# Optimization experiments

Hardware: AMD Instinct MI355X
Metric: run time of the kernel (lower is better)

## Reference

```python
import jax, jax.numpy as jnp
import numpy as np

ATT_PROP = 2  # config['att_prop']
NEG_BIAS = 1e23


def _bucket(d):
    # standard coref-style distance bucketing into 10 buckets
    d = jnp.abs(d)
    return jnp.where(d <= 4, d,
           jnp.where(d <= 7, 5,
           jnp.where(d <= 15, 6,
           jnp.where(d <= 31, 7,
           jnp.where(d <= 63, 8, 9))))).astype(jnp.int32)


def setup_inputs() -> dict:
    key = jax.random.key(0)
    ks = jax.random.split(key, 12)
    B, N, M, D, H = 2, 1024, 2048, 512, 64
    scale = 0.02  # init_weights_std

    update = jax.random.normal(ks[0], (B, N, D), jnp.float32)
    span_begin = jnp.sort(jax.random.randint(ks[1], (B, N), 0, 2000), axis=-1).astype(jnp.int32)
    span_end = (span_begin + jax.random.randint(ks[2], (B, N), 0, 10)).astype(jnp.int32)
    square_mask = jnp.ones((B, N, N), jnp.float32)
    cand_span_vecs = jax.random.normal(ks[3], (B, M, D), jnp.float32)
    # unique prune indices per batch (a pruned span maps to one candidate slot)
    prune_indices_hoi = jnp.stack([
        jnp.sort(jax.random.permutation(jax.random.fold_in(ks[4], b), M)[:N])
        for b in range(B)]).astype(jnp.int32)
    span_lengths = jnp.array([900, 1024], dtype=jnp.int32)

    W_left = jax.random.normal(ks[5], (D, H), jnp.float32) * scale
    W_right = jax.random.normal(ks[6], (D, H), jnp.float32) * scale
    b_h = jnp.zeros((H,), jnp.float32)
    dist_emb = jax.random.normal(ks[7], (10, H), jnp.float32) * scale
    v_out = jax.random.normal(ks[8], (H,), jnp.float32) * scale
    b_out = jnp.zeros((), jnp.float32)
    W_gate = jax.random.normal(ks[9], (2 * D, D), jnp.float32) * scale
    b_gate = jnp.zeros((D,), jnp.float32)

    return dict(update=update, square_mask=square_mask, cand_span_vecs=cand_span_vecs,
                span_begin=span_begin, span_end=span_end,
                prune_indices_hoi=prune_indices_hoi, span_lengths=span_lengths,
                W_left=W_left, W_right=W_right, b_h=b_h, dist_emb=dist_emb,
                v_out=v_out, b_out=b_out, W_gate=W_gate, b_gate=b_gate)


def reference(update, square_mask, cand_span_vecs, span_begin, span_end,
              prune_indices_hoi, span_lengths, W_left, W_right, b_h,
              dist_emb, v_out, b_out, W_gate, b_gate):
    B, N, D = update.shape
    # pairwise distance features are iteration-invariant: precompute once
    dist = dist_emb[_bucket(span_begin[:, :, None] - span_begin[:, None, :])]  # [B,N,N,H]
    bias = -(1.0 - square_mask) * NEG_BIAS  # [B,N,N]

    for _ in range(ATT_PROP):
        left = update @ W_left    # [B,N,H]
        right = update @ W_right  # [B,N,H]
        h = jax.nn.relu(left[:, :, None, :] + right[:, None, :, :] + dist + b_h)  # [B,N,N,H]
        scores = jnp.einsum('bijh,h->bij', h, v_out) + b_out  # [B,N,N]
        probs = jax.nn.softmax(scores + bias, axis=-1)
        ctxt = jnp.einsum('bij,bjd->bid', probs, update)  # [B,N,D]
        g = jax.nn.sigmoid(jnp.concatenate([update, ctxt], axis=-1) @ W_gate + b_gate)
        update = g * update + (1.0 - g) * ctxt

    # overwrite_spans_hoi: scatter first span_lengths[b] updated vectors back
    valid = jnp.arange(N) < span_lengths[:, None]  # [B,N]

    def scatter_one(cand, idx, upd, m):
        cur = cand[idx]  # [N,D]
        vals = jnp.where(m[:, None], upd, cur)  # invalid rows write back original
        return cand.at[idx].set(vals)

    cand_new = jax.vmap(scatter_one)(cand_span_vecs, prune_indices_hoi, update, valid)
    return cand_new, update
```

## Files before the change

kernel.cpp:

```cpp
#include <hip/hip_runtime.h>
#include <cstdint>

#define NB 2
#define NN 1024
#define MM 2048
#define DD 512
#define HH 64
#define ST 68
#define STB 72

typedef __attribute__((ext_vector_type(8))) short bf16x8;
typedef __attribute__((ext_vector_type(4))) float f32x4;

__device__ inline ushort f2bf(float x) {
  union { float f; uint32_t u; } v; v.f = x;
  uint32_t u = v.u;
  u += 0x7FFF + ((u >> 16) & 1);
  return (ushort)(u >> 16);
}
__device__ inline float bflo(uint32_t d) { return __uint_as_float(d << 16); }
__device__ inline float bfhi(uint32_t d) { return __uint_as_float(d & 0xFFFF0000u); }

#define GLDS(gp, lp) \
  __builtin_amdgcn_global_load_lds( \
      (const __attribute__((address_space(1))) void*)(gp), \
      (__attribute__((address_space(3))) void*)(lp), 16, 0, 0)

__global__ __launch_bounds__(256) void lr_kernel(
    const float* __restrict__ U, const float* __restrict__ Wl,
    const float* __restrict__ Wr, float* __restrict__ left,
    ushort* __restrict__ right_bf) {
  __shared__ float u[8][DD];
  const int block = blockIdx.x;
  const int tid = threadIdx.x;
  const float4* Uv = (const float4*)(U + (size_t)block * 8 * DD);
  float4* uv = (float4*)&u[0][0];
#pragma unroll
  for (int t = 0; t < 4; ++t) uv[tid + t * 256] = Uv[tid + t * 256];
  __syncthreads();
  const int h = tid & 63;
  const int isR = (tid >> 6) & 1;
  const int rbase = tid >> 7;
  const float* __restrict__ W = isR ? Wr : Wl;
  float acc[4] = {0.f, 0.f, 0.f, 0.f};
  for (int k0 = 0; k0 < DD; k0 += 4) {
    float w0 = W[(k0 + 0) * HH + h];
    float w1 = W[(k0 + 1) * HH + h];
    float w2 = W[(k0 + 2) * HH + h];
    float w3 = W[(k0 + 3) * HH + h];
#pragma unroll
    for (int r = 0; r < 4; ++r) {
      float4 u4 = *(const float4*)&u[rbase + r * 2][k0];
      acc[r] = fmaf(u4.w, w3, fmaf(u4.z, w2, fmaf(u4.y, w1, fmaf(u4.x, w0, acc[r]))));
    }
  }
  if (isR) {
#pragma unroll
    for (int r = 0; r < 4; ++r)
      right_bf[(size_t)(block * 8 + rbase + r * 2) * HH + h] = f2bf(acc[r]);
  } else {
#pragma unroll
    for (int r = 0; r < 4; ++r)
      left[(size_t)(block * 8 + rbase + r * 2) * HH + h] = acc[r];
  }
}

__global__ __launch_bounds__(256) void conv_t(
    const float* __restrict__ in, ushort* __restrict__ out_row,
    ushort* __restrict__ out_T, int R, int C, int write_row) {
  __shared__ float tile[64][65];
  const int b = blockIdx.z;
  const int r0 = blockIdx.y * 64, c0 = blockIdx.x * 64;
  const int tx = threadIdx.x & 15, ty = threadIdx.x >> 4;
  const float* inb = in + (size_t)b * R * C;
#pragma unroll
  for (int p = 0; p < 4; ++p) {
    const int r = ty + p * 16;
    const float4 v = *(const float4*)&inb[(size_t)(r0 + r) * C + c0 + tx * 4];
    tile[r][tx * 4 + 0] = v.x; tile[r][tx * 4 + 1] = v.y;
    tile[r][tx * 4 + 2] = v.z; tile[r][tx * 4 + 3] = v.w;
    if (write_row) {
      ushort4 o = make_ushort4(f2bf(v.x), f2bf(v.y), f2bf(v.z), f2bf(v.w));
      *(ushort4*)&out_row[(size_t)b * R * C + (size_t)(r0 + r) * C + c0 + tx * 4] = o;
    }
  }
  __syncthreads();
  ushort* oT = out_T + (size_t)b * R * C;
#pragma unroll
  for (int p = 0; p < 4; ++p) {
    const int rr = ty + p * 16;
    ushort4 o;
    o.x = f2bf(tile[tx * 4 + 0][rr]);
    o.y = f2bf(tile[tx * 4 + 1][rr]);
    o.z = f2bf(tile[tx * 4 + 2][rr]);
    o.w = f2bf(tile[tx * 4 + 3][rr]);
    *(ushort4*)&oT[(size_t)(c0 + rr) * R + r0 + tx * 4] = o;
  }
}

__global__ __launch_bounds__(256) void score_softmax(
    const float* __restrict__ left, const ushort* __restrict__ right_bf,
    const int* __restrict__ span_begin, const float* __restrict__ mask,
    const float* __restrict__ dist_emb, const float* __restrict__ b_h,
    const float* __restrict__ v_out, ushort* __restrict__ probs_bf) {
  __shared__ ushort Rt[64][STB];
  __shared__ ushort LDb[4][10][STB];
  __shared__ float Dbh[10][ST];
  __shared__ float Lt[4][ST];
  __shared__ float Sc[4][NN];
  __shared__ int sbj[NN];
  const int b = blockIdx.y;
  const int r0 = blockIdx.x * 4;
  const int tid = threadIdx.x;
  const int wave = tid >> 6, lane = tid & 63;
  const int row = r0 + wave;

  for (int f = tid; f < 160; f += 256) {
    int bk = f >> 4, h4 = f & 15;
    float4 d = *(const float4*)&dist_emb[bk * HH + h4 * 4];
    float4 bh = *(const float4*)&b_h[h4 * 4];
    d.x += bh.x; d.y += bh.y; d.z += bh.z; d.w += bh.w;
    *(float4*)&Dbh[bk][h4 * 4] = d;
  }
  if (tid < 64) {
    int r = tid >> 4, h4 = tid & 15;
    *(float4*)&Lt[r][h4 * 4] =
        *(const float4*)&left[((size_t)b * NN + r0 + r) * HH + h4 * 4];
  }
  for (int t = tid; t < NN; t += 256) sbj[t] = span_begin[b * NN + t];
  __syncthreads();
  for (int f = tid; f < 2560; f += 256) {
    int i = f >> 9;
    i = f / 640;
    int rem = f - i * 640;
    int bk = rem >> 6, h = rem & 63;
    LDb[i][bk][h] = f2bf(Lt[i][h] + Dbh[bk][h]);
  }
  float4 vr[16];
#pragma unroll
  for (int hq = 0; hq < 16; ++hq) vr[hq] = *(const float4*)&v_out[hq * 4];
  const int my_sbi = span_begin[(size_t)b * NN + row];
  const float* maskrow = mask + ((size_t)b * NN + row) * NN;

#pragma unroll 1
  for (int c = 0; c < 16; ++c) {
    __syncthreads();
#pragma unroll
    for (int t = 0; t < 2; ++t) {
      const int f = tid + t * 256;
      const int r = f >> 3, u8 = f & 7;
      *(bf16x8*)&Rt[r][u8 * 8] =
          *(const bf16x8*)&right_bf[((size_t)b * NN + c * 64 + r) * HH + u8 * 8];
    }
    __syncthreads();
    int d = sbj[c * 64 + lane] - my_sbi;
    d = d < 0 ? -d : d;
    const int bk =
        d <= 4 ? d : (d <= 7 ? 5 : (d <= 15 ? 6 : (d <= 31 ? 7 : (d <= 63 ? 8 : 9))));
    const ushort* zp = &LDb[wave][bk][0];
    const ushort* rp = &Rt[lane][0];
    float acc = 0.f;
#pragma unroll
    for (int oct = 0; oct < 8; ++oct) {
      const uint4 zd = *(const uint4*)&zp[oct * 8];
      const uint4 rd = *(const uint4*)&rp[oct * 8];
      const float4 v0 = vr[2 * oct], v1 = vr[2 * oct + 1];
      acc = fmaf(fmaxf(bflo(zd.x) + bflo(rd.x), 0.f), v0.x, acc);
      acc = fmaf(fmaxf(bfhi(zd.x) + bfhi(rd.x), 0.f), v0.y, acc);
      acc = fmaf(fmaxf(bflo(zd.y) + bflo(rd.y), 0.f), v0.z, acc);
      acc = fmaf(fmaxf(bfhi(zd.y) + bfhi(rd.y), 0.f), v0.w, acc);
      acc = fmaf(fmaxf(bflo(zd.z) + bflo(rd.z), 0.f), v1.x, acc);
      acc = fmaf(fmaxf(bfhi(zd.z) + bfhi(rd.z), 0.f), v1.y, acc);
      acc = fmaf(fmaxf(bflo(zd.w) + bflo(rd.w), 0.f), v1.z, acc);
      acc = fmaf(fmaxf(bfhi(zd.w) + bfhi(rd.w), 0.f), v1.w, acc);
    }
    const float mval = maskrow[c * 64 + lane];
    Sc[wave][c * 64 + lane] = acc - (1.0f - mval) * 1e23f;
  }
  float mx = -3.0e38f;
#pragma unroll
  for (int c = 0; c < 16; ++c) mx = fmaxf(mx, Sc[wave][c * 64 + lane]);
#pragma unroll
  for (int off = 32; off; off >>= 1) mx = fmaxf(mx, __shfl_xor(mx, off));
  float sum = 0.f;
#pragma unroll
  for (int c = 0; c < 16; ++c) {
    const float e = __expf(Sc[wave][c * 64 + lane] - mx);
    Sc[wave][c * 64 + lane] = e;
    sum += e;
  }
#pragma unroll
  for (int off = 32; off; off >>= 1) sum += __shfl_xor(sum, off);
  const float inv = 1.0f / sum;
  ushort* prow = probs_bf + ((size_t)b * NN + row) * NN;
#pragma unroll
  for (int c = 0; c < 16; ++c)
    prow[c * 64 + lane] = f2bf(Sc[wave][c * 64 + lane] * inv);
}

__global__ __launch_bounds__(256) void gemm_ctxt_mfma(
    const ushort* __restrict__ Pbf, const ushort* __restrict__ UT,
    ushort* __restrict__ Cbf) {
  __shared__ ushort As[64 * 64];
  __shared__ ushort Bs[64 * 64];
  const int b = blockIdx.z;
  const int m0 = blockIdx.y * 64, n0 = blockIdx.x * 64;
  const int tid = threadIdx.x;
  const int lane = tid & 63, wave = tid >> 6;
  const int wm = (wave >> 1) * 32, wn = (wave & 1) * 32;
  const ushort* Ab = Pbf + (size_t)b * NN * NN;
  const ushort* Bb = UT + (size_t)b * DD * NN;
  f32x4 acc[2][2] = {};
  const int fm = lane & 15, quad = lane >> 4;
  for (int k0 = 0; k0 < NN; k0 += 64) {
#pragma unroll
    for (int t = 0; t < 2; ++t) {
      const int idx = tid + t * 256;
      const int r = idx >> 3, c8 = idx & 7;
      const int g = c8 ^ (r & 7);
      GLDS(Ab + (size_t)(m0 + r) * NN + k0 + g * 8, As + idx * 8);
      GLDS(Bb + (size_t)(n0 + r) * NN + k0 + g * 8, Bs + idx * 8);
    }
    __syncthreads();
#pragma unroll
    for (int s = 0; s < 2; ++s) {
      bf16x8 af[2], bfr[2];
#pragma unroll
      for (int tm = 0; tm < 2; ++tm) {
        const int row = wm + tm * 16 + fm;
        const int c8 = (s * 4 + quad) ^ (row & 7);
        af[tm] = *(const bf16x8*)&As[row * 64 + c8 * 8];
      }
#pragma unroll
      for (int tn = 0; tn < 2; ++tn) {
        const int row = wn + tn * 16 + fm;
        const int c8 = (s * 4 + quad) ^ (row & 7);
        bfr[tn] = *(const bf16x8*)&Bs[row * 64 + c8 * 8];
      }
#pragma unroll
      for (int tm = 0; tm < 2; ++tm)
#pragma unroll
        for (int tn = 0; tn < 2; ++tn)
          acc[tm][tn] = __builtin_amdgcn_mfma_f32_16x16x32_bf16(
              af[tm], bfr[tn], acc[tm][tn], 0, 0, 0);
    }
    __syncthreads();
  }
#pragma unroll
  for (int tm = 0; tm < 2; ++tm)
#pragma unroll
    for (int tn = 0; tn < 2; ++tn) {
      const int col = n0 + wn + tn * 16 + fm;
#pragma unroll
      for (int r = 0; r < 4; ++r) {
        const int row = m0 + wm + tm * 16 + quad * 4 + r;
        Cbf[(size_t)b * NN * DD + (size_t)row * DD + col] = f2bf(acc[tm][tn][r]);
      }
    }
}

__global__ __launch_bounds__(256) void gemm_gate_mfma(
    const ushort* __restrict__ Ubf, const ushort* __restrict__ Cbf,
    const ushort* __restrict__ WgT, const float* __restrict__ bg,
    const float* __restrict__ Uf, float* __restrict__ Uout,
    ushort* __restrict__ UbfOut, ushort* __restrict__ UTOut) {
  __shared__ ushort As[64 * 64];
  __shared__ ushort Bs[64 * 64];
  __shared__ ushort Tt[64][66];
  const int b = blockIdx.z;
  const int m0 = blockIdx.y * 64, n0 = blockIdx.x * 64;
  const int tid = threadIdx.x;
  const int lane = tid & 63, wave = tid >> 6;
  const int wm = (wave >> 1) * 32, wn = (wave & 1) * 32;
  f32x4 acc[2][2] = {};
  const int fm = lane & 15, quad = lane >> 4;
  for (int k0 = 0; k0 < 2 * DD; k0 += 64) {
    const ushort* Abase = (k0 < DD) ? (Ubf + (size_t)b * NN * DD)
                                    : (Cbf + (size_t)b * NN * DD);
    const int kc = k0 & (DD - 1);
#pragma unroll
    for (int t = 0; t < 2; ++t) {
      const int idx = tid + t * 256;
      const int r = idx >> 3, c8 = idx & 7;
      const int g = c8 ^ (r & 7);
      GLDS(Abase + (size_t)(m0 + r) * DD + kc + g * 8, As + idx * 8);
      GLDS(WgT + (size_t)(n0 + r) * (2 * DD) + k0 + g * 8, Bs + idx * 8);
    }
    __syncthreads();
#pragma unroll
    for (int s = 0; s < 2; ++s) {
      bf16x8 af[2], bfr[2];
#pragma unroll
      for (int tm = 0; tm < 2; ++tm) {
        const int row = wm + tm * 16 + fm;
        const int c8 = (s * 4 + quad) ^ (row & 7);
        af[tm] = *(const bf16x8*)&As[row * 64 + c8 * 8];
      }
#pragma unroll
      for (int tn = 0; tn < 2; ++tn) {
        const int row = wn + tn * 16 + fm;
        const int c8 = (s * 4 + quad) ^ (row & 7);
        bfr[tn] = *(const bf16x8*)&Bs[row * 64 + c8 * 8];
      }
#pragma unroll
      for (int tm = 0; tm < 2; ++tm)
#pragma unroll
        for (int tn = 0; tn < 2; ++tn)
          acc[tm][tn] = __builtin_amdgcn_mfma_f32_16x16x32_bf16(
              af[tm], bfr[tn], acc[tm][tn], 0, 0, 0);
    }
    __syncthreads();
  }
#pragma unroll
  for (int tm = 0; tm < 2; ++tm)
#pragma unroll
    for (int tn = 0; tn < 2; ++tn) {
      const int cl = wn + tn * 16 + fm;
      const int col = n0 + cl;
      const float bgv = bg[col];
#pragma unroll
      for (int r = 0; r < 4; ++r) {
        const int rl = wm + tm * 16 + quad * 4 + r;
        const int row = m0 + rl;
        const size_t off = (size_t)b * NN * DD + (size_t)row * DD + col;
        const float g = 1.f / (1.f + __expf(-(acc[tm][tn][r] + bgv)));
        const float cv = __uint_as_float(((uint32_t)Cbf[off]) << 16);
        const float o = g * Uf[off] + (1.f - g) * cv;
        Uout[off] = o;
        const ushort ob = f2bf(o);
        UbfOut[off] = ob;
        Tt[rl][cl] = ob;
      }
    }
  __syncthreads();
#pragma unroll
  for (int p = 0; p < 4; ++p) {
    const int cl = (tid >> 4) + p * 16;
    const int rl = (tid & 15) * 4;
    ushort4 o;
    o.x = Tt[rl + 0][cl]; o.y = Tt[rl + 1][cl];
    o.z = Tt[rl + 2][cl]; o.w = Tt[rl + 3][cl];
    *(ushort4*)&UTOut[((size_t)b * DD + n0 + cl) * NN + m0 + rl] = o;
  }
}

__global__ __launch_bounds__(256) void out_copy(
    const float* __restrict__ cand, const float* __restrict__ upd,
    float* __restrict__ out) {
  const int t = blockIdx.x * 256 + threadIdx.x;
  float4* o4 = (float4*)out;
  if (t < 524288) o4[t] = ((const float4*)cand)[t];
  else o4[t] = ((const float4*)upd)[t - 524288];
}

__global__ __launch_bounds__(128) void scatter_k(
    float* __restrict__ out_cand, const float* __restrict__ upd,
    const int* __restrict__ prune, const int* __restrict__ span_len) {
  const int row = blockIdx.x;
  const int b = row >> 10, i = row & 1023;
  if (i >= span_len[b]) return;
  const int dst = prune[row];
  const float4* src = (const float4*)(upd + (size_t)row * DD);
  float4* d = (float4*)(out_cand + ((size_t)b * MM + dst) * DD);
  d[threadIdx.x] = src[threadIdx.x];
}

extern "C" void kernel_launch(void* const* d_in, const int* in_sizes, int n_in,
                              void* d_out, int out_size, void* d_ws, size_t ws_size,
                              hipStream_t stream) {
  const float* update = (const float*)d_in[0];
  const float* mask = (const float*)d_in[1];
  const float* cand = (const float*)d_in[2];
  const int* span_begin = (const int*)d_in[3];
  const int* prune = (const int*)d_in[5];
  const int* span_len = (const int*)d_in[6];
  const float* Wl = (const float*)d_in[7];
  const float* Wr = (const float*)d_in[8];
  const float* b_h = (const float*)d_in[9];
  const float* dist_emb = (const float*)d_in[10];
  const float* v_out = (const float*)d_in[11];
  const float* Wg = (const float*)d_in[13];
  const float* b_gate = (const float*)d_in[14];

  char* w = (char*)d_ws;
  float* left = (float*)w;        w += (size_t)NB * NN * HH * 4;
  ushort* right_bf = (ushort*)w;  w += (size_t)NB * NN * HH * 2;
  ushort* probs_bf = (ushort*)w;  w += (size_t)NB * NN * NN * 2;
  ushort* ctxt_bf = (ushort*)w;   w += (size_t)NB * NN * DD * 2;
  float* upd1 = (float*)w;        w += (size_t)NB * NN * DD * 4;
  float* upd2 = (float*)w;        w += (size_t)NB * NN * DD * 4;
  ushort* Ubf0 = (ushort*)w;      w += (size_t)NB * NN * DD * 2;
  ushort* Ubf1 = (ushort*)w;      w += (size_t)NB * NN * DD * 2;
  ushort* UT = (ushort*)w;        w += (size_t)NB * NN * DD * 2;
  ushort* WgT = (ushort*)w;       w += (size_t)2 * DD * DD * 2;

  float* out = (float*)d_out;

  conv_t<<<dim3(8, 16, 1), 256, 0, stream>>>(Wg, WgT, WgT, 2 * DD, DD, 0);
  conv_t<<<dim3(8, 16, NB), 256, 0, stream>>>(update, Ubf0, UT, NN, DD, 1);

  const float* Ucur = update;
  float* nexts[2] = {upd1, upd2};
  ushort* ubf_in[2] = {Ubf0, Ubf1};
  ushort* ubf_out[2] = {Ubf1, Ubf0};
  for (int it = 0; it < 2; ++it) {
    lr_kernel<<<256, 256, 0, stream>>>(Ucur, Wl, Wr, left, right_bf);
    score_softmax<<<dim3(NN / 4, NB), 256, 0, stream>>>(
        left, right_bf, span_begin, mask, dist_emb, b_h, v_out, probs_bf);
    gemm_ctxt_mfma<<<dim3(8, 16, NB), 256, 0, stream>>>(probs_bf, UT, ctxt_bf);
    gemm_gate_mfma<<<dim3(8, 16, NB), 256, 0, stream>>>(
        ubf_in[it], ctxt_bf, WgT, b_gate, Ucur, nexts[it], ubf_out[it], UT);
    Ucur = nexts[it];
  }
  out_copy<<<3072, 256, 0, stream>>>(cand, Ucur, out);
  scatter_k<<<NB * NN, 128, 0, stream>>>(out, Ucur, prune, span_len);
}
```

Before: 240.1 us.

## Fuse all stages into one persistent kernel with software grid barriers

Replaces the sequence of separate launches (transpose/convert, left-right projection, score softmax, context GEMM, gate GEMM, copy, scatter) with a single persistent kernel of 512 blocks that walks the phases and separates them with an atomic-counter grid barrier. The aim is to remove per-launch overhead and the idle gaps between small kernels. The candidate copy is overlapped with the first projection phase, and the score dot product is split into two accumulators for more instruction-level parallelism. In exchange, all 512 blocks must be co-resident for the barrier to avoid deadlock, the GEMM phases use only 256 of the 512 blocks, and each barrier costs spinning on atomics.

Result: slower. 913.8 us (+280.6%).

```diff
diff --git a/kernel.cpp b/kernel.cpp
--- a/kernel.cpp
+++ b/kernel.cpp
@@ -8,6 +8,7 @@
 #define HH 64
 #define ST 68
 #define STB 72
+#define GRID 512
 
 typedef __attribute__((ext_vector_type(8))) short bf16x8;
 typedef __attribute__((ext_vector_type(4))) float f32x4;
@@ -26,66 +27,52 @@
       (const __attribute__((address_space(1))) void*)(gp), \
       (__attribute__((address_space(3))) void*)(lp), 16, 0, 0)
 
-__global__ __launch_bounds__(256) void lr_kernel(
-    const float* __restrict__ U, const float* __restrict__ Wl,
-    const float* __restrict__ Wr, float* __restrict__ left,
-    ushort* __restrict__ right_bf) {
-  __shared__ float u[8][DD];
-  const int block = blockIdx.x;
-  const int tid = threadIdx.x;
-  const float4* Uv = (const float4*)(U + (size_t)block * 8 * DD);
-  float4* uv = (float4*)&u[0][0];
-#pragma unroll
-  for (int t = 0; t < 4; ++t) uv[tid + t * 256] = Uv[tid + t * 256];
-  __syncthreads();
-  const int h = tid & 63;
-  const int isR = (tid >> 6) & 1;
-  const int rbase = tid >> 7;
-  const float* __restrict__ W = isR ? Wr : Wl;
-  float acc[4] = {0.f, 0.f, 0.f, 0.f};
-  for (int k0 = 0; k0 < DD; k0 += 4) {
-    float w0 = W[(k0 + 0) * HH + h];
-    float w1 = W[(k0 + 1) * HH + h];
-    float w2 = W[(k0 + 2) * HH + h];
-    float w3 = W[(k0 + 3) * HH + h];
-#pragma unroll
-    for (int r = 0; r < 4; ++r) {
-      float4 u4 = *(const float4*)&u[rbase + r * 2][k0];
-      acc[r] = fmaf(u4.w, w3, fmaf(u4.z, w2, fmaf(u4.y, w1, fmaf(u4.x, w0, acc[r]))));
-    }
-  }
-  if (isR) {
-#pragma unroll
-    for (int r = 0; r < 4; ++r)
-      right_bf[(size_t)(block * 8 + rbase + r * 2) * HH + h] = f2bf(acc[r]);
-  } else {
-#pragma unroll
-    for (int r = 0; r < 4; ++r)
-      left[(size_t)(block * 8 + rbase + r * 2) * HH + h] = acc[r];
-  }
-}
-
-__global__ __launch_bounds__(256) void conv_t(
-    const float* __restrict__ in, ushort* __restrict__ out_row,
-    ushort* __restrict__ out_T, int R, int C, int write_row) {
-  __shared__ float tile[64][65];
-  const int b = blockIdx.z;
-  const int r0 = blockIdx.y * 64, c0 = blockIdx.x * 64;
+struct KP {
+  const float *update, *mask, *cand;
+  const int *span_begin, *prune, *span_len;
+  const float *Wl, *Wr, *b_h, *dist_emb, *v_out, *Wg, *b_gate;
+  float *out;
+  int *bar;
+  float *left; ushort *right_bf; ushort *probs_bf; ushort *ctxt_bf;
+  float *upd1, *upd2; ushort *Ubf0, *Ubf1, *UT, *WgT;
+};
+
+__device__ inline void gsync(int* bar) {
+  __syncthreads();
+  __threadfence();
+  if (threadIdx.x == 0) {
+    int* cnt = bar;
+    int* gen = bar + 1;
+    const int g = atomicAdd(gen, 0);
+    if (atomicAdd(cnt, 1) == GRID - 1) {
+      atomicExch(cnt, 0);
+      __threadfence();
+      atomicAdd(gen, 1);
+    } else {
+      while (atomicAdd(gen, 0) == g) __builtin_amdgcn_s_sleep(2);
+    }
+    __threadfence();
+  }
+  __syncthreads();
+}
+
+__device__ void conv_tile(const float* __restrict__ in, ushort* out_row,
+                          ushort* __restrict__ out_T, int R, int C,
+                          int r0, int c0, char* smem) {
+  float (*tile)[65] = (float(*)[65])smem;
   const int tx = threadIdx.x & 15, ty = threadIdx.x >> 4;
-  const float* inb = in + (size_t)b * R * C;
 #pragma unroll
   for (int p = 0; p < 4; ++p) {
     const int r = ty + p * 16;
-    const float4 v = *(const float4*)&inb[(size_t)(r0 + r) * C + c0 + tx * 4];
+    const float4 v = *(const float4*)&in[(size_t)(r0 + r) * C + c0 + tx * 4];
     tile[r][tx * 4 + 0] = v.x; tile[r][tx * 4 + 1] = v.y;
     tile[r][tx * 4 + 2] = v.z; tile[r][tx * 4 + 3] = v.w;
-    if (write_row) {
+    if (out_row) {
       ushort4 o = make_ushort4(f2bf(v.x), f2bf(v.y), f2bf(v.z), f2bf(v.w));
-      *(ushort4*)&out_row[(size_t)b * R * C + (size_t)(r0 + r) * C + c0 + tx * 4] = o;
-    }
-  }
-  __syncthreads();
-  ushort* oT = out_T + (size_t)b * R * C;
+      *(ushort4*)&out_row[(size_t)(r0 + r) * C + c0 + tx * 4] = o;
+    }
+  }
+  __syncthreads();
 #pragma unroll
   for (int p = 0; p < 4; ++p) {
     const int rr = ty + p * 16;
@@ -94,53 +81,86 @@
     o.y = f2bf(tile[tx * 4 + 1][rr]);
     o.z = f2bf(tile[tx * 4 + 2][rr]);
     o.w = f2bf(tile[tx * 4 + 3][rr]);
-    *(ushort4*)&oT[(size_t)(c0 + rr) * R + r0 + tx * 4] = o;
-  }
-}
-
-__global__ __launch_bounds__(256) void score_softmax(
-    const float* __restrict__ left, const ushort* __restrict__ right_bf,
-    const int* __restrict__ span_begin, const float* __restrict__ mask,
-    const float* __restrict__ dist_emb, const float* __restrict__ b_h,
-    const float* __restrict__ v_out, ushort* __restrict__ probs_bf) {
-  __shared__ ushort Rt[64][STB];
-  __shared__ ushort LDb[4][10][STB];
-  __shared__ float Dbh[10][ST];
-  __shared__ float Lt[4][ST];
-  __shared__ float Sc[4][NN];
-  __shared__ int sbj[NN];
-  const int b = blockIdx.y;
-  const int r0 = blockIdx.x * 4;
+    *(ushort4*)&out_T[(size_t)(c0 + rr) * R + r0 + tx * 4] = o;
+  }
+  __syncthreads();
+}
+
+__device__ void lr_phase(const KP& P, const float* __restrict__ U, int vb,
+                         char* smem) {
+  float (*u)[DD] = (float(*)[DD])smem;
+  const int tid = threadIdx.x;
+  const float4* Uv = (const float4*)(U + (size_t)vb * 4 * DD);
+  float4* uv = (float4*)&u[0][0];
+#pragma unroll
+  for (int t = 0; t < 2; ++t) uv[tid + t * 256] = Uv[tid + t * 256];
+  __syncthreads();
+  const int h = tid & 63;
+  const int isR = (tid >> 6) & 1;
+  const int rsel = tid >> 7;
+  const float* __restrict__ W = isR ? P.Wr : P.Wl;
+  float acc[2] = {0.f, 0.f};
+  for (int k0 = 0; k0 < DD; k0 += 4) {
+    float w0 = W[(k0 + 0) * HH + h];
+    float w1 = W[(k0 + 1) * HH + h];
+    float w2 = W[(k0 + 2) * HH + h];
+    float w3 = W[(k0 + 3) * HH + h];
+#pragma unroll
+    for (int r = 0; r < 2; ++r) {
+      float4 u4 = *(const float4*)&u[rsel + r * 2][k0];
+      acc[r] = fmaf(u4.w, w3, fmaf(u4.z, w2, fmaf(u4.y, w1, fmaf(u4.x, w0, acc[r]))));
+    }
+  }
+  if (isR) {
+#pragma unroll
+    for (int r = 0; r < 2; ++r)
+      P.right_bf[(size_t)(vb * 4 + rsel + r * 2) * HH + h] = f2bf(acc[r]);
+  } else {
+#pragma unroll
+    for (int r = 0; r < 2; ++r)
+      P.left[(size_t)(vb * 4 + rsel + r * 2) * HH + h] = acc[r];
+  }
+  __syncthreads();
+}
+
+__device__ void score_phase(const KP& P, int vb, char* smem) {
+  ushort (*Rt)[STB] = (ushort(*)[STB])(smem);
+  ushort (*LDb)[10][STB] = (ushort(*)[10][STB])(smem + 9216);
+  float (*Dbh)[ST] = (float(*)[ST])(smem + 14976);
+  float (*Lt)[ST] = (float(*)[ST])(smem + 17696);
+  float (*Sc)[NN] = (float(*)[NN])(smem + 18784);
+  int* sbj = (int*)(smem + 35168);
+  const int b = vb >> 8;
+  const int r0 = (vb & 255) * 4;
   const int tid = threadIdx.x;
   const int wave = tid >> 6, lane = tid & 63;
   const int row = r0 + wave;
 
   for (int f = tid; f < 160; f += 256) {
     int bk = f >> 4, h4 = f & 15;
-    float4 d = *(const float4*)&dist_emb[bk * HH + h4 * 4];
-    float4 bh = *(const float4*)&b_h[h4 * 4];
+    float4 d = *(const float4*)&P.dist_emb[bk * HH + h4 * 4];
+    float4 bh = *(const float4*)&P.b_h[h4 * 4];
     d.x += bh.x; d.y += bh.y; d.z += bh.z; d.w += bh.w;
     *(float4*)&Dbh[bk][h4 * 4] = d;
   }
   if (tid < 64) {
     int r = tid >> 4, h4 = tid & 15;
     *(float4*)&Lt[r][h4 * 4] =
-        *(const float4*)&left[((size_t)b * NN + r0 + r) * HH + h4 * 4];
-  }
-  for (int t = tid; t < NN; t += 256) sbj[t] = span_begin[b * NN + t];
+        *(const float4*)&P.left[((size_t)b * NN + r0 + r) * HH + h4 * 4];
+  }
+  for (int t = tid; t < NN; t += 256) sbj[t] = P.span_begin[b * NN + t];
   __syncthreads();
   for (int f = tid; f < 2560; f += 256) {
-    int i = f >> 9;
-    i = f / 640;
+    int i = f / 640;
     int rem = f - i * 640;
     int bk = rem >> 6, h = rem & 63;
     LDb[i][bk][h] = f2bf(Lt[i][h] + Dbh[bk][h]);
   }
   float4 vr[16];
 #pragma unroll
-  for (int hq = 0; hq < 16; ++hq) vr[hq] = *(const float4*)&v_out[hq * 4];
-  const int my_sbi = span_begin[(size_t)b * NN + row];
-  const float* maskrow = mask + ((size_t)b * NN + row) * NN;
+  for (int hq = 0; hq < 16; ++hq) vr[hq] = *(const float4*)&P.v_out[hq * 4];
+  const int my_sbi = P.span_begin[(size_t)b * NN + row];
+  const float* maskrow = P.mask + ((size_t)b * NN + row) * NN;
 
 #pragma unroll 1
   for (int c = 0; c < 16; ++c) {
@@ -150,7 +170,7 @@
       const int f = tid + t * 256;
       const int r = f >> 3, u8 = f & 7;
       *(bf16x8*)&Rt[r][u8 * 8] =
-          *(const bf16x8*)&right_bf[((size_t)b * NN + c * 64 + r) * HH + u8 * 8];
+          *(const bf16x8*)&P.right_bf[((size_t)b * NN + c * 64 + r) * HH + u8 * 8];
     }
     __syncthreads();
     int d = sbj[c * 64 + lane] - my_sbi;
@@ -159,23 +179,38 @@
         d <= 4 ? d : (d <= 7 ? 5 : (d <= 15 ? 6 : (d <= 31 ? 7 : (d <= 63 ? 8 : 9))));
     const ushort* zp = &LDb[wave][bk][0];
     const ushort* rp = &Rt[lane][0];
-    float acc = 0.f;
-#pragma unroll
-    for (int oct = 0; oct < 8; ++oct) {
-      const uint4 zd = *(const uint4*)&zp[oct * 8];
-      const uint4 rd = *(const uint4*)&rp[oct * 8];
-      const float4 v0 = vr[2 * oct], v1 = vr[2 * oct + 1];
-      acc = fmaf(fmaxf(bflo(zd.x) + bflo(rd.x), 0.f), v0.x, acc);
-      acc = fmaf(fmaxf(bfhi(zd.x) + bfhi(rd.x), 0.f), v0.y, acc);
-      acc = fmaf(fmaxf(bflo(zd.y) + bflo(rd.y), 0.f), v0.z, acc);
-      acc = fmaf(fmaxf(bfhi(zd.y) + bfhi(rd.y), 0.f), v0.w, acc);
-      acc = fmaf(fmaxf(bflo(zd.z) + bflo(rd.z), 0.f), v1.x, acc);
-      acc = fmaf(fmaxf(bfhi(zd.z) + bfhi(rd.z), 0.f), v1.y, acc);
-      acc = fmaf(fmaxf(bflo(zd.w) + bflo(rd.w), 0.f), v1.z, acc);
-      acc = fmaf(fmaxf(bfhi(zd.w) + bfhi(rd.w), 0.f), v1.w, acc);
+    float acc0 = 0.f, acc1 = 0.f;
+#pragma unroll
+    for (int oct = 0; oct < 8; oct += 2) {
+      {
+        const uint4 zd = *(const uint4*)&zp[oct * 8];
+        const uint4 rd = *(const uint4*)&rp[oct * 8];
+        const float4 v0 = vr[2 * oct], v1 = vr[2 * oct + 1];
+        acc0 = fmaf(fmaxf(bflo(zd.x) + bflo(rd.x), 0.f), v0.x, acc0);
+        acc0 = fmaf(fmaxf(bfhi(zd.x) + bfhi(rd.x), 0.f), v0.y, acc0);
+        acc0 = fmaf(fmaxf(bflo(zd.y) + bflo(rd.y), 0.f), v0.z, acc0);
+        acc0 = fmaf(fmaxf(bfhi(zd.y) + bfhi(rd.y), 0.f), v0.w, acc0);
+        acc0 = fmaf(fmaxf(bflo(zd.z) + bflo(rd.z), 0.f), v1.x, acc0);
+        acc0 = fmaf(fmaxf(bfhi(zd.z) + bfhi(rd.z), 0.f), v1.y, acc0);
+        acc0 = fmaf(fmaxf(bflo(zd.w) + bflo(rd.w), 0.f), v1.z, acc0);
+        acc0 = fmaf(fmaxf(bfhi(zd.w) + bfhi(rd.w), 0.f), v1.w, acc0);
+      }
+      {
+        const uint4 zd = *(const uint4*)&zp[(oct + 1) * 8];
+        const uint4 rd = *(const uint4*)&rp[(oct + 1) * 8];
+        const float4 v0 = vr[2 * oct + 2], v1 = vr[2 * oct + 3];
+        acc1 = fmaf(fmaxf(bflo(zd.x) + bflo(rd.x), 0.f), v0.x, acc1);
+        acc1 = fmaf(fmaxf(bfhi(zd.x) + bfhi(rd.x), 0.f), v0.y, acc1);
+        acc1 = fmaf(fmaxf(bflo(zd.y) + bflo(rd.y), 0.f), v0.z, acc1);
+        acc1 = fmaf(fmaxf(bfhi(zd.y) + bfhi(rd.y), 0.f), v0.w, acc1);
+        acc1 = fmaf(fmaxf(bflo(zd.z) + bflo(rd.z), 0.f), v1.x, acc1);
+        acc1 = fmaf(fmaxf(bfhi(zd.z) + bfhi(rd.z), 0.f), v1.y, acc1);
+        acc1 = fmaf(fmaxf(bflo(zd.w) + bflo(rd.w), 0.f), v1.z, acc1);
+        acc1 = fmaf(fmaxf(bfhi(zd.w) + bfhi(rd.w), 0.f), v1.w, acc1);
+      }
     }
     const float mval = maskrow[c * 64 + lane];
-    Sc[wave][c * 64 + lane] = acc - (1.0f - mval) * 1e23f;
+    Sc[wave][c * 64 + lane] = (acc0 + acc1) - (1.0f - mval) * 1e23f;
   }
   float mx = -3.0e38f;
 #pragma unroll
@@ -192,24 +227,24 @@
 #pragma unroll
   for (int off = 32; off; off >>= 1) sum += __shfl_xor(sum, off);
   const float inv = 1.0f / sum;
-  ushort* prow = probs_bf + ((size_t)b * NN + row) * NN;
+  ushort* prow = P.probs_bf + ((size_t)b * NN + row) * NN;
 #pragma unroll
   for (int c = 0; c < 16; ++c)
     prow[c * 64 + lane] = f2bf(Sc[wave][c * 64 + lane] * inv);
-}
-
-__global__ __launch_bounds__(256) void gemm_ctxt_mfma(
-    const ushort* __restrict__ Pbf, const ushort* __restrict__ UT,
-    ushort* __restrict__ Cbf) {
-  __shared__ ushort As[64 * 64];
-  __shared__ ushort Bs[64 * 64];
-  const int b = blockIdx.z;
-  const int m0 = blockIdx.y * 64, n0 = blockIdx.x * 64;
+  __syncthreads();
+}
+
+__device__ void ctxt_phase(const KP& P, int vb, char* smem) {
+  ushort* As = (ushort*)smem;
+  ushort* Bs = (ushort*)(smem + 8192);
+  const int b = vb >> 7;
+  const int rem = vb & 127;
+  const int m0 = (rem >> 3) * 64, n0 = (rem & 7) * 64;
   const int tid = threadIdx.x;
   const int lane = tid & 63, wave = tid >> 6;
   const int wm = (wave >> 1) * 32, wn = (wave & 1) * 32;
-  const ushort* Ab = Pbf + (size_t)b * NN * NN;
-  const ushort* Bb = UT + (size_t)b * DD * NN;
+  const ushort* Ab = P.probs_bf + (size_t)b * NN * NN;
+  const ushort* Bb = P.UT + (size_t)b * DD * NN;
   f32x4 acc[2][2] = {};
   const int fm = lane & 15, quad = lane >> 4;
   for (int k0 = 0; k0 < NN; k0 += 64) {
@@ -254,21 +289,20 @@
 #pragma unroll
       for (int r = 0; r < 4; ++r) {
         const int row = m0 + wm + tm * 16 + quad * 4 + r;
-        Cbf[(size_t)b * NN * DD + (size_t)row * DD + col] = f2bf(acc[tm][tn][r]);
-      }
-    }
-}
-
-__global__ __launch_bounds__(256) void gemm_gate_mfma(
-    const ushort* __restrict__ Ubf, const ushort* __restrict__ Cbf,
-    const ushort* __restrict__ WgT, const float* __restrict__ bg,
-    const float* __restrict__ Uf, float* __restrict__ Uout,
-    ushort* __restrict__ UbfOut, ushort* __restrict__ UTOut) {
-  __shared__ ushort As[64 * 64];
-  __shared__ ushort Bs[64 * 64];
-  __shared__ ushort Tt[64][66];
-  const int b = blockIdx.z;
-  const int m0 = blockIdx.y * 64, n0 = blockIdx.x * 64;
+        P.ctxt_bf[(size_t)b * NN * DD + (size_t)row * DD + col] = f2bf(acc[tm][tn][r]);
+      }
+    }
+}
+
+__device__ void gate_phase(const KP& P, const ushort* __restrict__ Ubf,
+                           const float* __restrict__ Uf, float* __restrict__ Uout,
+                           ushort* __restrict__ UbfOut, int vb, char* smem) {
+  ushort* As = (ushort*)smem;
+  ushort* Bs = (ushort*)(smem + 8192);
+  ushort (*Tt)[66] = (ushort(*)[66])(smem + 16384);
+  const int b = vb >> 7;
+  const int rem = vb & 127;
+  const int m0 = (rem >> 3) * 64, n0 = (rem & 7) * 64;
   const int tid = threadIdx.x;
   const int lane = tid & 63, wave = tid >> 6;
   const int wm = (wave >> 1) * 32, wn = (wave & 1) * 32;
@@ -276,7 +310,7 @@
   const int fm = lane & 15, quad = lane >> 4;
   for (int k0 = 0; k0 < 2 * DD; k0 += 64) {
     const ushort* Abase = (k0 < DD) ? (Ubf + (size_t)b * NN * DD)
-                                    : (Cbf + (size_t)b * NN * DD);
+                                    : (P.ctxt_bf + (size_t)b * NN * DD);
     const int kc = k0 & (DD - 1);
 #pragma unroll
     for (int t = 0; t < 2; ++t) {
@@ -284,7 +318,7 @@
       const int r = idx >> 3, c8 = idx & 7;
       const int g = c8 ^ (r & 7);
       GLDS(Abase + (size_t)(m0 + r) * DD + kc + g * 8, As + idx * 8);
-      GLDS(WgT + (size_t)(n0 + r) * (2 * DD) + k0 + g * 8, Bs + idx * 8);
+      GLDS(P.WgT + (size_t)(n0 + r) * (2 * DD) + k0 + g * 8, Bs + idx * 8);
     }
     __syncthreads();
 #pragma unroll
@@ -317,14 +351,14 @@
     for (int tn = 0; tn < 2; ++tn) {
       const int cl = wn + tn * 16 + fm;
       const int col = n0 + cl;
-      const float bgv = bg[col];
+      const float bgv = P.b_gate[col];
 #pragma unroll
       for (int r = 0; r < 4; ++r) {
         const int rl = wm + tm * 16 + quad * 4 + r;
         const int row = m0 + rl;
         const size_t off = (size_t)b * NN * DD + (size_t)row * DD + col;
         const float g = 1.f / (1.f + __expf(-(acc[tm][tn][r] + bgv)));
-        const float cv = __uint_as_float(((uint32_t)Cbf[off]) << 16);
+        const float cv = __uint_as_float(((uint32_t)P.ctxt_bf[off]) << 16);
         const float o = g * Uf[off] + (1.f - g) * cv;
         Uout[off] = o;
         const ushort ob = f2bf(o);
@@ -340,78 +374,102 @@
     ushort4 o;
     o.x = Tt[rl + 0][cl]; o.y = Tt[rl + 1][cl];
     o.z = Tt[rl + 2][cl]; o.w = Tt[rl + 3][cl];
-    *(ushort4*)&UTOut[((size_t)b * DD + n0 + cl) * NN + m0 + rl] = o;
-  }
-}
-
-__global__ __launch_bounds__(256) void out_copy(
-    const float* __restrict__ cand, const float* __restrict__ upd,
-    float* __restrict__ out) {
-  const int t = blockIdx.x * 256 + threadIdx.x;
-  float4* o4 = (float4*)out;
-  if (t < 524288) o4[t] = ((const float4*)cand)[t];
-  else o4[t] = ((const float4*)upd)[t - 524288];
-}
-
-__global__ __launch_bounds__(128) void scatter_k(
-    float* __restrict__ out_cand, const float* __restrict__ upd,
-    const int* __restrict__ prune, const int* __restrict__ span_len) {
-  const int row = blockIdx.x;
-  const int b = row >> 10, i = row & 1023;
-  if (i >= span_len[b]) return;
-  const int dst = prune[row];
-  const float4* src = (const float4*)(upd + (size_t)row * DD);
-  float4* d = (float4*)(out_cand + ((size_t)b * MM + dst) * DD);
-  d[threadIdx.x] = src[threadIdx.x];
+    *(ushort4*)&P.UT[((size_t)b * DD + n0 + cl) * NN + m0 + rl] = o;
+  }
+  __syncthreads();
+}
+
+__global__ __launch_bounds__(256, 2) void fused_all(KP P) {
+  __shared__ __align__(16) char smem[39264];
+  const int bid = blockIdx.x;
+  const int tid = threadIdx.x;
+
+  for (int vb = bid; vb < 384; vb += GRID) {
+    if (vb < 128) {
+      conv_tile(P.Wg, nullptr, P.WgT, 2 * DD, DD, (vb >> 3) * 64, (vb & 7) * 64,
+                smem);
+    } else {
+      const int t = vb - 128, b = t >> 7, rem = t & 127;
+      conv_tile(P.update + (size_t)b * NN * DD, P.Ubf0 + (size_t)b * NN * DD,
+                P.UT + (size_t)b * DD * NN, NN, DD, (rem >> 3) * 64,
+                (rem & 7) * 64, smem);
+    }
+  }
+  lr_phase(P, P.update, bid, smem);
+  {
+    const float4* c4 = (const float4*)P.cand;
+    float4* o4 = (float4*)P.out;
+    for (int idx = bid * 256 + tid; idx < NB * MM * DD / 4; idx += GRID * 256)
+      o4[idx] = c4[idx];
+  }
+  gsync(P.bar);
+
+  for (int it = 0; it < 2; ++it) {
+    score_phase(P, bid, smem);
+    gsync(P.bar);
+    if (bid < 256) ctxt_phase(P, bid, smem);
+    gsync(P.bar);
+    const float* Uf = it ? P.upd1 : P.update;
+    float* Uout = it ? P.upd2 : P.upd1;
+    const ushort* Ubf_in = it ? P.Ubf1 : P.Ubf0;
+    ushort* Ubf_out = it ? P.Ubf0 : P.Ubf1;
+    if (bid < 256) gate_phase(P, Ubf_in, Uf, Uout, Ubf_out, bid, smem);
+    gsync(P.bar);
+    if (it == 0) {
+      lr_phase(P, P.upd1, bid, smem);
+      gsync(P.bar);
+    }
+  }
+
+  {
+    const float4* u4 = (const float4*)P.upd2;
+    float4* o4 = (float4*)P.out + (size_t)NB * MM * DD / 4;
+    for (int idx = bid * 256 + tid; idx < NB * NN * DD / 4; idx += GRID * 256)
+      o4[idx] = u4[idx];
+    for (int row = bid; row < NB * NN; row += GRID) {
+      const int b = row >> 10, i = row & 1023;
+      if (i < P.span_len[b] && tid < 128) {
+        const int dst = P.prune[row];
+        const float4* src = (const float4*)(P.upd2 + (size_t)row * DD);
+        float4* d = (float4*)(P.out + ((size_t)b * MM + dst) * DD);
+        d[tid] = src[tid];
+      }
+    }
+  }
 }
 
 extern "C" void kernel_launch(void* const* d_in, const int* in_sizes, int n_in,
                               void* d_out, int out_size, void* d_ws, size_t ws_size,
                               hipStream_t stream) {
-  const float* update = (const float*)d_in[0];
-  const float* mask = (const float*)d_in[1];
-  const float* cand = (const float*)d_in[2];
-  const int* span_begin = (const int*)d_in[3];
-  const int* prune = (const int*)d_in[5];
-  const int* span_len = (const int*)d_in[6];
-  const float* Wl = (const float*)d_in[7];
-  const float* Wr = (const float*)d_in[8];
-  const float* b_h = (const float*)d_in[9];
-  const float* dist_emb = (const float*)d_in[10];
-  const float* v_out = (const float*)d_in[11];
-  const float* Wg = (const float*)d_in[13];
-  const float* b_gate = (const float*)d_in[14];
+  KP p;
+  p.update = (const float*)d_in[0];
+  p.mask = (const float*)d_in[1];
+  p.cand = (const float*)d_in[2];
+  p.span_begin = (const int*)d_in[3];
+  p.prune = (const int*)d_in[5];
+  p.span_len = (const int*)d_in[6];
+  p.Wl = (const float*)d_in[7];
+  p.Wr = (const float*)d_in[8];
+  p.b_h = (const float*)d_in[9];
+  p.dist_emb = (const float*)d_in[10];
+  p.v_out = (const float*)d_in[11];
+  p.Wg = (const float*)d_in[13];
+  p.b_gate = (const float*)d_in[14];
+  p.out = (float*)d_out;
 
   char* w = (char*)d_ws;
-  float* left = (float*)w;        w += (size_t)NB * NN * HH * 4;
-  ushort* right_bf = (ushort*)w;  w += (size_t)NB * NN * HH * 2;
-  ushort* probs_bf = (ushort*)w;  w += (size_t)NB * NN * NN * 2;
-  ushort* ctxt_bf = (ushort*)w;   w += (size_t)NB * NN * DD * 2;
-  float* upd1 = (float*)w;        w += (size_t)NB * NN * DD * 4;
-  float* upd2 = (float*)w;        w += (size_t)NB * NN * DD * 4;
-  ushort* Ubf0 = (ushort*)w;      w += (size_t)NB * NN * DD * 2;
-  ushort* Ubf1 = (ushort*)w;      w += (size_t)NB * NN * DD * 2;
-  ushort* UT = (ushort*)w;        w += (size_t)NB * NN * DD * 2;
-  ushort* WgT = (ushort*)w;       w += (size_t)2 * DD * DD * 2;
-
-  float* out = (float*)d_out;
-
-  conv_t<<<dim3(8, 16, 1), 256, 0, stream>>>(Wg, WgT, WgT, 2 * DD, DD, 0);
-  conv_t<<<dim3(8, 16, NB), 256, 0, stream>>>(update, Ubf0, UT, NN, DD, 1);
-
-  const float* Ucur = update;
-  float* nexts[2] = {upd1, upd2};
-  ushort* ubf_in[2] = {Ubf0, Ubf1};
-  ushort* ubf_out[2] = {Ubf1, Ubf0};
-  for (int it = 0; it < 2; ++it) {
-    lr_kernel<<<256, 256, 0, stream>>>(Ucur, Wl, Wr, left, right_bf);
-    score_softmax<<<dim3(NN / 4, NB), 256, 0, stream>>>(
-        left, right_bf, span_begin, mask, dist_emb, b_h, v_out, probs_bf);
-    gemm_ctxt_mfma<<<dim3(8, 16, NB), 256, 0, stream>>>(probs_bf, UT, ctxt_bf);
-    gemm_gate_mfma<<<dim3(8, 16, NB), 256, 0, stream>>>(
-        ubf_in[it], ctxt_bf, WgT, b_gate, Ucur, nexts[it], ubf_out[it], UT);
-    Ucur = nexts[it];
-  }
-  out_copy<<<3072, 256, 0, stream>>>(cand, Ucur, out);
-  scatter_k<<<NB * NN, 128, 0, stream>>>(out, Ucur, prune, span_len);
-}
+  p.bar = (int*)w;         w += 256;
+  p.left = (float*)w;      w += (size_t)NB * NN * HH * 4;
+  p.right_bf = (ushort*)w; w += (size_t)NB * NN * HH * 2;
+  p.probs_bf = (ushort*)w; w += (size_t)NB * NN * NN * 2;
+  p.ctxt_bf = (ushort*)w;  w += (size_t)NB * NN * DD * 2;
+  p.upd1 = (float*)w;      w += (size_t)NB * NN * DD * 4;
+  p.upd2 = (float*)w;      w += (size_t)NB * NN * DD * 4;
+  p.Ubf0 = (ushort*)w;     w += (size_t)NB * NN * DD * 2;
+  p.Ubf1 = (ushort*)w;     w += (size_t)NB * NN * DD * 2;
+  p.UT = (ushort*)w;       w += (size_t)NB * NN * DD * 2;
+  p.WgT = (ushort*)w;      w += (size_t)2 * DD * DD * 2;
+
+  hipMemsetAsync(d_ws, 0, 256, stream);
+  fused_all<<<dim3(GRID), dim3(256), 0, stream>>>(p);
+}
```
